# Kernel optimization log

Hardware: AMD Instinct MI355X
Metric: run time of the kernel (lower is better)

## Reference

```python
import jax, jax.numpy as jnp
import numpy as np

THRESHOLD = 1.0


def setup_inputs() -> dict:
    key = jax.random.key(0)
    ks = jax.random.split(key, 7)
    B, D = 262144, 128
    U1, U2 = 64, 32
    return {
        "x": jax.random.normal(ks[0], (B, D), dtype=jnp.float32),
        "W1": jax.random.normal(ks[1], (U1, D), dtype=jnp.float32) * 0.05,
        "b1": jax.random.normal(ks[2], (U1,), dtype=jnp.float32) * 0.05,
        "W2": jax.random.normal(ks[3], (U2, D), dtype=jnp.float32) * 0.05,
        "b2": jax.random.normal(ks[4], (U2,), dtype=jnp.float32) * 0.05,
        "Wf": jax.random.normal(ks[5], (D, U1), dtype=jnp.float32) * 0.05,
        "bf": jax.random.normal(ks[6], (D,), dtype=jnp.float32) * 0.05,
    }


def reference(x, W1, b1, W2, b2, Wf, bf):
    # Per-sample routing decision: mean |x_i| > threshold -> branch1 else branch2
    mask = jnp.mean(jnp.abs(x), axis=1) > THRESHOLD  # (B,)
    o1 = jax.nn.relu(x @ W1.T + b1)                  # (B, 64)
    o2 = jax.nn.relu(x @ W2.T + b2)                  # (B, 32)
    final_dim = W1.shape[0]                          # max(64, 32) = 64
    o2p = jnp.pad(o2, ((0, 0), (0, final_dim - o2.shape[1])))  # zero-pad to final_dim
    branch_out = jnp.where(mask[:, None], o1, o2p)   # (B, 64)
    return branch_out @ Wf.T + bf                    # (B, 128)
```

## Files before the change

### kernel.cpp

```cpp
#include <hip/hip_runtime.h>
#include <stdint.h>

#define FLAG_THRESH 127.0f

typedef short bfrag __attribute__((ext_vector_type(8)));
typedef float floatx4 __attribute__((ext_vector_type(4)));
typedef int intx4 __attribute__((ext_vector_type(4)));

__device__ __forceinline__ unsigned bf16pk(float a, float b) {
    unsigned ua = __float_as_uint(a), ub = __float_as_uint(b);
    ua = (ua + 0x7fffu + ((ua >> 16) & 1u)) >> 16;
    ub = (ub + 0x7fffu + ((ub >> 16) & 1u)) & 0xffff0000u;
    return ua | ub;
}
__device__ __forceinline__ unsigned short bf16s(float a) {
    unsigned ua = __float_as_uint(a);
    return (unsigned short)((ua + 0x7fffu + ((ua >> 16) & 1u)) >> 16);
}
__device__ __forceinline__ bfrag mkfrag(unsigned a, unsigned b, unsigned c, unsigned d) {
    intx4 v = {(int)a, (int)b, (int)c, (int)d};
    return __builtin_bit_cast(bfrag, v);
}
__device__ __forceinline__ void lds_fence_wave() {
    __builtin_amdgcn_wave_barrier();
    __builtin_amdgcn_s_waitcnt(0xc07f);
    __builtin_amdgcn_wave_barrier();
}

__global__ __launch_bounds__(256, 4)
void dyn_main(const float* __restrict__ x, const float* __restrict__ W1,
              const float* __restrict__ b1, const float* __restrict__ W2,
              const float* __restrict__ b2, const float* __restrict__ Wf,
              const float* __restrict__ bf, float* __restrict__ out,
              int ntiles)
{
    __shared__ __align__(16) short w2f[8][64][8];
    __shared__ __align__(16) short wff[8][64][8];
    __shared__ __align__(16) float bfl[128];
    __shared__ __align__(16) short hbuf[4][16 * 40];
    __shared__ __align__(16) float xr[4][128];
    __shared__ __align__(16) float hh[4][64];

    const int tid  = threadIdx.x;
    const int wave = tid >> 6, lane = tid & 63;
    const int l15  = lane & 15, q = lane >> 4;

    for (int idx = tid; idx < 4096; idx += 256) {
        const int j = idx & 7, ln = (idx >> 3) & 63, blk = idx >> 9;
        const int ks = blk >> 1, nb = blk & 1;
        const int u = nb * 16 + (ln & 15);
        const int k = ks * 32 + ((ln >> 4) << 3) + j;
        ((short*)w2f)[idx] = (short)bf16s(W2[u * 128 + k]);
        const int d = blk * 16 + (ln & 15);
        const int c = ((ln >> 4) << 3) + j;
        ((short*)wff)[idx] = (short)bf16s(Wf[d * 64 + c]);
    }
    for (int i = tid; i < 128; i += 256) bfl[i] = bf[i];
    const float b2r0 = b2[l15], b2r1 = b2[16 + l15];
    __syncthreads();

    const unsigned ov = (l15 == 0) ? 0x3f803f80u : 0u;
    const bfrag onesf = mkfrag(ov, ov, ov, ov);

    const int wid = blockIdx.x * 4 + wave;
    const int wstride = gridDim.x * 4;

    long long cur = wid;
    bool more = cur < ntiles;
    floatx4 xl[8];
    if (more) {
        const float* base = x + cur * 2048 + l15 * 128 + q * 8;
        #pragma unroll
        for (int ks = 0; ks < 4; ++ks) {
            xl[2 * ks]     = *(const floatx4*)(base + ks * 32);
            xl[2 * ks + 1] = *(const floatx4*)(base + ks * 32 + 4);
        }
    }

    while (more) {
        const long long nxt = cur + wstride;
        const bool hasnxt = nxt < ntiles;
        floatx4 xc[8];
        #pragma unroll
        for (int i = 0; i < 8; ++i) xc[i] = xl[i];
        if (hasnxt) {
            const float* base = x + nxt * 2048 + l15 * 128 + q * 8;
            #pragma unroll
            for (int ks = 0; ks < 4; ++ks) {
                xl[2 * ks]     = *(const floatx4*)(base + ks * 32);
                xl[2 * ks + 1] = *(const floatx4*)(base + ks * 32 + 4);
            }
        }

        floatx4 a0 = {0.f, 0.f, 0.f, 0.f}, a1 = a0, asum = a0;
        #pragma unroll
        for (int ks = 0; ks < 4; ++ks) {
            const floatx4 p = xc[2 * ks], r = xc[2 * ks + 1];
            const unsigned u0 = bf16pk(p[0], p[1]), u1 = bf16pk(p[2], p[3]);
            const unsigned u2 = bf16pk(r[0], r[1]), u3 = bf16pk(r[2], r[3]);
            const bfrag af = mkfrag(u0, u1, u2, u3);
            const bfrag aa = mkfrag(u0 & 0x7fff7fffu, u1 & 0x7fff7fffu,
                                    u2 & 0x7fff7fffu, u3 & 0x7fff7fffu);
            const bfrag w0 = *(const bfrag*)&w2f[ks * 2 + 0][lane][0];
            const bfrag w1 = *(const bfrag*)&w2f[ks * 2 + 1][lane][0];
            a0   = __builtin_amdgcn_mfma_f32_16x16x32_bf16(af, w0, a0, 0, 0, 0);
            a1   = __builtin_amdgcn_mfma_f32_16x16x32_bf16(af, w1, a1, 0, 0, 0);
            asum = __builtin_amdgcn_mfma_f32_16x16x32_bf16(aa, onesf, asum, 0, 0, 0);
        }

        unsigned rowmask = 0;
        #pragma unroll
        for (int reg = 0; reg < 4; ++reg) {
            const unsigned long long bm =
                __ballot(l15 == 0 && asum[reg] > FLAG_THRESH);
            rowmask |= (unsigned)( bm        & 1ull) << (0 + reg);
            rowmask |= (unsigned)((bm >> 16) & 1ull) << (4 + reg);
            rowmask |= (unsigned)((bm >> 32) & 1ull) << (8 + reg);
            rowmask |= (unsigned)((bm >> 48) & 1ull) << (12 + reg);
        }

        if (__builtin_expect(rowmask != 0, 0)) {
            unsigned m = rowmask;
            while (m) {
                const int r = (int)__builtin_ctz(m); m &= m - 1;
                if (l15 == r) {
                    #pragma unroll
                    for (int ks = 0; ks < 4; ++ks) {
                        *(floatx4*)&xr[wave][ks * 32 + q * 8]     = xc[2 * ks];
                        *(floatx4*)&xr[wave][ks * 32 + q * 8 + 4] = xc[2 * ks + 1];
                    }
                }
                lds_fence_wave();
                const float e0 = xr[wave][lane * 2], e1 = xr[wave][lane * 2 + 1];
                float s = fabsf(e0) + fabsf(e1);
                #pragma unroll
                for (int d = 1; d < 64; d <<= 1) s += __shfl_xor(s, d);
                float hv = 0.f;
                if (s > 128.0f) {
                    float a = 0.f;
                    for (int k = 0; k < 128; k += 4) {
                        const float4 qq = *(const float4*)&xr[wave][k];
                        const float4 wv = *(const float4*)&W1[lane * 128 + k];
                        a = fmaf(qq.x, wv.x, a); a = fmaf(qq.y, wv.y, a);
                        a = fmaf(qq.z, wv.z, a); a = fmaf(qq.w, wv.w, a);
                    }
                    hv = fmaxf(a + b1[lane], 0.f);
                } else if (lane < 32) {
                    float a = 0.f;
                    for (int k = 0; k < 128; k += 4) {
                        const float4 qq = *(const float4*)&xr[wave][k];
                        const float4 wv = *(const float4*)&W2[lane * 128 + k];
                        a = fmaf(qq.x, wv.x, a); a = fmaf(qq.y, wv.y, a);
                        a = fmaf(qq.z, wv.z, a); a = fmaf(qq.w, wv.w, a);
                    }
                    hv = fmaxf(a + b2[lane], 0.f);
                }
                hh[wave][lane] = hv;
                lds_fence_wave();
                #pragma unroll
                for (int jj = 0; jj < 2; ++jj) {
                    const int d = lane + 64 * jj;
                    float a = bf[d];
                    for (int u = 0; u < 64; ++u)
                        a = fmaf(hh[wave][u], Wf[d * 64 + u], a);
                    out[(cur * 16 + r) * 128 + d] = a;
                }
                lds_fence_wave();
            }
        }

        short* hb = &hbuf[wave][0];
        #pragma unroll
        for (int reg = 0; reg < 4; ++reg) {
            const int row = q * 4 + reg;
            hb[row * 40 + l15]      = (short)bf16s(fmaxf(a0[reg] + b2r0, 0.f));
            hb[row * 40 + 16 + l15] = (short)bf16s(fmaxf(a1[reg] + b2r1, 0.f));
        }

        lds_fence_wave();

        const bfrag hfrag = *(const bfrag*)&hb[l15 * 40 + q * 8];
        floatx4 o[8];
        #pragma unroll
        for (int mb = 0; mb < 8; ++mb) o[mb] = (floatx4){0.f, 0.f, 0.f, 0.f};
        #pragma unroll
        for (int mb = 0; mb < 8; ++mb) {
            const bfrag wfr = *(const bfrag*)&wff[mb][lane][0];
            o[mb] = __builtin_amdgcn_mfma_f32_16x16x32_bf16(wfr, hfrag, o[mb], 0, 0, 0);
        }

        float* obase = out + (cur * 16 + l15) * 128 + q * 4;
        if (__builtin_expect(rowmask == 0, 1)) {
            #pragma unroll
            for (int mb = 0; mb < 8; ++mb) {
                const floatx4 bv = *(const floatx4*)&bfl[mb * 16 + q * 4];
                const floatx4 v = o[mb] + bv;
                *(floatx4*)(obase + mb * 16) = v;
            }
        } else {
            if (((rowmask >> l15) & 1u) == 0u) {
                #pragma unroll
                for (int mb = 0; mb < 8; ++mb) {
                    const floatx4 bv = *(const floatx4*)&bfl[mb * 16 + q * 4];
                    const floatx4 v = o[mb] + bv;
                    *(floatx4*)(obase + mb * 16) = v;
                }
            }
        }

        lds_fence_wave();
        cur = nxt; more = hasnxt;
    }
}

extern "C" void kernel_launch(void* const* d_in, const int* in_sizes, int n_in,
                              void* d_out, int out_size, void* d_ws, size_t ws_size,
                              hipStream_t stream) {
    const float* x  = (const float*)d_in[0];
    const float* W1 = (const float*)d_in[1];
    const float* b1 = (const float*)d_in[2];
    const float* W2 = (const float*)d_in[3];
    const float* b2 = (const float*)d_in[4];
    const float* Wf = (const float*)d_in[5];
    const float* bf = (const float*)d_in[6];
    float* out = (float*)d_out;
    (void)d_ws; (void)ws_size;

    const int B = in_sizes[0] / 128;
    const int ntiles = B / 16;

    hipLaunchKernelGGL(dyn_main, dim3(1024), dim3(256), 0, stream,
                       x, W1, b1, W2, b2, Wf, bf, out, ntiles);
}
```

Measured before the change: 262.2 us.

## Stream x tiles into swizzled LDS via async global_load_lds double buffering

Replaces register prefetch of x with direct global-to-LDS 16-byte async loads into a per-wave double buffer using an XOR swizzle, with explicit vmcnt waits. Blocks grow to 512 threads (8 waves) and the grid shrinks to 256 blocks. The fallback path for rows above the threshold now reads x from the LDS buffer, and the bf16 output is always written first and then overwritten for flagged rows. This frees VGPRs and aims to keep more loads in flight, at the cost of 128KB+ of LDS per block, which limits occupancy, and an extra store for flagged rows.

```diff
diff --git a/kernel.cpp b/kernel.cpp
--- a/kernel.cpp
+++ b/kernel.cpp
@@ -27,25 +27,41 @@
     __builtin_amdgcn_wave_barrier();
 }
 
-__global__ __launch_bounds__(256, 4)
+#define VM0  0x0F70
+#define VM8  0x0F78
+#define VM16 0x4F70
+#define WAITVM(imm) do {                       \
+    asm volatile("" ::: "memory");             \
+    __builtin_amdgcn_s_waitcnt(imm);           \
+    asm volatile("" ::: "memory");             \
+    __builtin_amdgcn_sched_barrier(0);         \
+} while (0)
+
+__device__ __forceinline__ void gl16(const void* gsrc, void* ldst) {
+    __builtin_amdgcn_global_load_lds(
+        (const __attribute__((address_space(1))) unsigned int*)gsrc,
+        (__attribute__((address_space(3))) unsigned int*)ldst, 16, 0, 0);
+}
+
+__global__ __launch_bounds__(512, 2)
 void dyn_main(const float* __restrict__ x, const float* __restrict__ W1,
               const float* __restrict__ b1, const float* __restrict__ W2,
               const float* __restrict__ b2, const float* __restrict__ Wf,
               const float* __restrict__ bf, float* __restrict__ out,
               int ntiles)
 {
+    __shared__ __align__(16) float xbuf[8][2][2048];
     __shared__ __align__(16) short w2f[8][64][8];
     __shared__ __align__(16) short wff[8][64][8];
     __shared__ __align__(16) float bfl[128];
-    __shared__ __align__(16) short hbuf[4][16 * 40];
-    __shared__ __align__(16) float xr[4][128];
-    __shared__ __align__(16) float hh[4][64];
+    __shared__ __align__(16) short hbuf[8][16 * 40];
+    __shared__ __align__(16) float hh[8][64];
 
     const int tid  = threadIdx.x;
     const int wave = tid >> 6, lane = tid & 63;
     const int l15  = lane & 15, q = lane >> 4;
 
-    for (int idx = tid; idx < 4096; idx += 256) {
+    for (int idx = tid; idx < 4096; idx += 512) {
         const int j = idx & 7, ln = (idx >> 3) & 63, blk = idx >> 9;
         const int ks = blk >> 1, nb = blk & 1;
         const int u = nb * 16 + (ln & 15);
@@ -55,47 +71,51 @@
         const int c = ((ln >> 4) << 3) + j;
         ((short*)wff)[idx] = (short)bf16s(Wf[d * 64 + c]);
     }
-    for (int i = tid; i < 128; i += 256) bfl[i] = bf[i];
+    for (int i = tid; i < 128; i += 512) bfl[i] = bf[i];
     const float b2r0 = b2[l15], b2r1 = b2[16 + l15];
     __syncthreads();
 
     const unsigned ov = (l15 == 0) ? 0x3f803f80u : 0u;
     const bfrag onesf = mkfrag(ov, ov, ov, ov);
 
-    const int wid = blockIdx.x * 4 + wave;
-    const int wstride = gridDim.x * 4;
+    const int wid = blockIdx.x * 8 + wave;
+    const int wstride = gridDim.x * 8;
+
+#define ISSUE_TILE(t, b) do {                                              \
+        const char* gb_ = (const char*)(x + (long long)(t) * 2048);        \
+        char* lb_ = (char*)&xbuf[wave][(b)][0];                            \
+        _Pragma("unroll")                                                  \
+        for (int j_ = 0; j_ < 8; ++j_) {                                   \
+            const int off_ = j_ * 1024 + lane * 16;                        \
+            const int src_ = off_ ^ (((off_ >> 9) & 7) << 4);              \
+            gl16(gb_ + src_, lb_ + j_ * 1024);                             \
+        }                                                                  \
+        __builtin_amdgcn_sched_barrier(0);                                 \
+    } while (0)
 
     long long cur = wid;
     bool more = cur < ntiles;
-    floatx4 xl[8];
-    if (more) {
-        const float* base = x + cur * 2048 + l15 * 128 + q * 8;
-        #pragma unroll
-        for (int ks = 0; ks < 4; ++ks) {
-            xl[2 * ks]     = *(const floatx4*)(base + ks * 32);
-            xl[2 * ks + 1] = *(const floatx4*)(base + ks * 32 + 4);
-        }
-    }
+    int bufc = 0;
+    if (more) ISSUE_TILE(cur, 0);
+    bool first = true;
 
     while (more) {
         const long long nxt = cur + wstride;
         const bool hasnxt = nxt < ntiles;
-        floatx4 xc[8];
-        #pragma unroll
-        for (int i = 0; i < 8; ++i) xc[i] = xl[i];
-        if (hasnxt) {
-            const float* base = x + nxt * 2048 + l15 * 128 + q * 8;
-            #pragma unroll
-            for (int ks = 0; ks < 4; ++ks) {
-                xl[2 * ks]     = *(const floatx4*)(base + ks * 32);
-                xl[2 * ks + 1] = *(const floatx4*)(base + ks * 32 + 4);
-            }
-        }
+        if (hasnxt) ISSUE_TILE(nxt, bufc ^ 1);
+
+        if (first) { if (hasnxt) WAITVM(VM8);  else WAITVM(VM0); }
+        else       { if (hasnxt) WAITVM(VM16); else WAITVM(VM8); }
+
+        const char* xb = (const char*)&xbuf[wave][bufc][0];
+        const int sw = (l15 & 7) << 4;
 
         floatx4 a0 = {0.f, 0.f, 0.f, 0.f}, a1 = a0, asum = a0;
         #pragma unroll
         for (int ks = 0; ks < 4; ++ks) {
-            const floatx4 p = xc[2 * ks], r = xc[2 * ks + 1];
+            const int g0 = (l15 << 9) + (ks << 7) + (q << 5);
+            const floatx4 p = *(const floatx4*)(xb + (g0 ^ sw));
+            const floatx4 r = *(const floatx4*)(xb + ((g0 + 16) ^ sw));
             const unsigned u0 = bf16pk(p[0], p[1]), u1 = bf16pk(p[2], p[3]);
             const unsigned u2 = bf16pk(r[0], r[1]), u3 = bf16pk(r[2], r[3]);
             const bfrag af = mkfrag(u0, u1, u2, u3);
@@ -119,27 +139,51 @@
             rowmask |= (unsigned)((bm >> 48) & 1ull) << (12 + reg);
         }
 
+        short* hb = &hbuf[wave][0];
+        #pragma unroll
+        for (int reg = 0; reg < 4; ++reg) {
+            const int row = q * 4 + reg;
+            hb[row * 40 + l15]      = (short)bf16s(fmaxf(a0[reg] + b2r0, 0.f));
+            hb[row * 40 + 16 + l15] = (short)bf16s(fmaxf(a1[reg] + b2r1, 0.f));
+        }
+
+        lds_fence_wave();
+
+        const bfrag hfrag = *(const bfrag*)&hb[l15 * 40 + q * 8];
+        floatx4 o[8];
+        #pragma unroll
+        for (int mb = 0; mb < 8; ++mb) o[mb] = (floatx4){0.f, 0.f, 0.f, 0.f};
+        #pragma unroll
+        for (int mb = 0; mb < 8; ++mb) {
+            const bfrag wfr = *(const bfrag*)&wff[mb][lane][0];
+            o[mb] = __builtin_amdgcn_mfma_f32_16x16x32_bf16(wfr, hfrag, o[mb], 0, 0, 0);
+        }
+
+        float* obase = out + (cur * 16 + l15) * 128 + q * 4;
+        #pragma unroll
+        for (int mb = 0; mb < 8; ++mb) {
+            const floatx4 bv = *(const floatx4*)&bfl[mb * 16 + q * 4];
+            const floatx4 v = o[mb] + bv;
+            *(floatx4*)(obase + mb * 16) = v;
+        }
+
         if (__builtin_expect(rowmask != 0, 0)) {
-            unsigned m = rowmask;
-            while (m) {
-                const int r = (int)__builtin_ctz(m); m &= m - 1;
-                if (l15 == r) {
-                    #pragma unroll
-                    for (int ks = 0; ks < 4; ++ks) {
-                        *(floatx4*)&xr[wave][ks * 32 + q * 8]     = xc[2 * ks];
-                        *(floatx4*)&xr[wave][ks * 32 + q * 8 + 4] = xc[2 * ks + 1];
-                    }
-                }
-                lds_fence_wave();
-                const float e0 = xr[wave][lane * 2], e1 = xr[wave][lane * 2 + 1];
-                float s = fabsf(e0) + fabsf(e1);
+            WAITVM(VM0);
+            unsigned mm = rowmask;
+            while (mm) {
+                const int r = (int)__builtin_ctz(mm); mm &= mm - 1;
+                const int swr = (r & 7) << 4;
+                const float2 xv =
+                    *(const float2*)(xb + (((r << 9) + lane * 8) ^ swr));
+                float s = fabsf(xv.x) + fabsf(xv.y);
                 #pragma unroll
                 for (int d = 1; d < 64; d <<= 1) s += __shfl_xor(s, d);
                 float hv = 0.f;
                 if (s > 128.0f) {
                     float a = 0.f;
                     for (int k = 0; k < 128; k += 4) {
-                        const float4 qq = *(const float4*)&xr[wave][k];
+                        const float4 qq = *(const float4*)(
+                            xb + (((r << 9) + (k << 2)) ^ swr));
                         const float4 wv = *(const float4*)&W1[lane * 128 + k];
                         a = fmaf(qq.x, wv.x, a); a = fmaf(qq.y, wv.y, a);
                         a = fmaf(qq.z, wv.z, a); a = fmaf(qq.w, wv.w, a);
@@ -148,7 +192,8 @@
                 } else if (lane < 32) {
                     float a = 0.f;
                     for (int k = 0; k < 128; k += 4) {
-                        const float4 qq = *(const float4*)&xr[wave][k];
+                        const float4 qq = *(const float4*)(
+                            xb + (((r << 9) + (k << 2)) ^ swr));
                         const float4 wv = *(const float4*)&W2[lane * 128 + k];
                         a = fmaf(qq.x, wv.x, a); a = fmaf(qq.y, wv.y, a);
                         a = fmaf(qq.z, wv.z, a); a = fmaf(qq.w, wv.w, a);
@@ -169,48 +214,10 @@
             }
         }
 
-        short* hb = &hbuf[wave][0];
-        #pragma unroll
-        for (int reg = 0; reg < 4; ++reg) {
-            const int row = q * 4 + reg;
-            hb[row * 40 + l15]      = (short)bf16s(fmaxf(a0[reg] + b2r0, 0.f));
-            hb[row * 40 + 16 + l15] = (short)bf16s(fmaxf(a1[reg] + b2r1, 0.f));
-        }
-
         lds_fence_wave();
-
-        const bfrag hfrag = *(const bfrag*)&hb[l15 * 40 + q * 8];
-        floatx4 o[8];
-        #pragma unroll
-        for (int mb = 0; mb < 8; ++mb) o[mb] = (floatx4){0.f, 0.f, 0.f, 0.f};
-        #pragma unroll
-        for (int mb = 0; mb < 8; ++mb) {
-            const bfrag wfr = *(const bfrag*)&wff[mb][lane][0];
-            o[mb] = __builtin_amdgcn_mfma_f32_16x16x32_bf16(wfr, hfrag, o[mb], 0, 0, 0);
-        }
-
-        float* obase = out + (cur * 16 + l15) * 128 + q * 4;
-        if (__builtin_expect(rowmask == 0, 1)) {
-            #pragma unroll
-            for (int mb = 0; mb < 8; ++mb) {
-                const floatx4 bv = *(const floatx4*)&bfl[mb * 16 + q * 4];
-                const floatx4 v = o[mb] + bv;
-                *(floatx4*)(obase + mb * 16) = v;
-            }
-        } else {
-            if (((rowmask >> l15) & 1u) == 0u) {
-                #pragma unroll
-                for (int mb = 0; mb < 8; ++mb) {
-                    const floatx4 bv = *(const floatx4*)&bfl[mb * 16 + q * 4];
-                    const floatx4 v = o[mb] + bv;
-                    *(floatx4*)(obase + mb * 16) = v;
-                }
-            }
-        }
-
-        lds_fence_wave();
-        cur = nxt; more = hasnxt;
+        first = false; bufc ^= 1; cur = nxt; more = hasnxt;
     }
+#undef ISSUE_TILE
 }
 
 extern "C" void kernel_launch(void* const* d_in, const int* in_sizes, int n_in,
@@ -229,6 +236,6 @@
     const int B = in_sizes[0] / 128;
     const int ntiles = B / 16;
 
-    hipLaunchKernelGGL(dyn_main, dim3(1024), dim3(256), 0, stream,
+    hipLaunchKernelGGL(dyn_main, dim3(256), dim3(512), 0, stream,
                        x, W1, b1, W2, b2, Wf, bf, out, ntiles);
 }
```

Result: faster. 255.7 us (-2.5%).

## Reorder rare-row fixup after main store, drop LDS staging, raise grid

Applied to the files above, without the earlier changes.

The fast MFMA path now runs unconditionally and writes all 16 rows. Any flagged rows are then recomputed in fp32 and overwritten, with a waitcnt placed first so the earlier stores are ordered before the overwrite. The xr/hh LDS arrays are removed: the fixup reads x directly from global memory and reuses hbuf as scratch, which cuts LDS use and may allow more blocks per CU. The grid grows from a fixed 1024 blocks to up to 2048, sized by tile count, which changes the persistent-block scheduling.

```diff
diff --git a/kernel.cpp b/kernel.cpp
--- a/kernel.cpp
+++ b/kernel.cpp
@@ -38,8 +38,6 @@
     __shared__ __align__(16) short wff[8][64][8];
     __shared__ __align__(16) float bfl[128];
     __shared__ __align__(16) short hbuf[4][16 * 40];
-    __shared__ __align__(16) float xr[4][128];
-    __shared__ __align__(16) float hh[4][64];
 
     const int tid  = threadIdx.x;
     const int wave = tid >> 6, lane = tid & 63;
@@ -119,27 +117,50 @@
             rowmask |= (unsigned)((bm >> 48) & 1ull) << (12 + reg);
         }
 
+        short* hb = &hbuf[wave][0];
+        #pragma unroll
+        for (int reg = 0; reg < 4; ++reg) {
+            const int row = q * 4 + reg;
+            hb[row * 40 + l15]      = (short)bf16s(fmaxf(a0[reg] + b2r0, 0.f));
+            hb[row * 40 + 16 + l15] = (short)bf16s(fmaxf(a1[reg] + b2r1, 0.f));
+        }
+
+        lds_fence_wave();
+
+        const bfrag hfrag = *(const bfrag*)&hb[l15 * 40 + q * 8];
+        floatx4 o[8];
+        #pragma unroll
+        for (int mb = 0; mb < 8; ++mb) o[mb] = (floatx4){0.f, 0.f, 0.f, 0.f};
+        #pragma unroll
+        for (int mb = 0; mb < 8; ++mb) {
+            const bfrag wfr = *(const bfrag*)&wff[mb][lane][0];
+            o[mb] = __builtin_amdgcn_mfma_f32_16x16x32_bf16(wfr, hfrag, o[mb], 0, 0, 0);
+        }
+
+        float* obase = out + (cur * 16 + l15) * 128 + q * 4;
+        #pragma unroll
+        for (int mb = 0; mb < 8; ++mb) {
+            const floatx4 bv = *(const floatx4*)&bfl[mb * 16 + q * 4];
+            const floatx4 v = o[mb] + bv;
+            *(floatx4*)(obase + mb * 16) = v;
+        }
+
         if (__builtin_expect(rowmask != 0, 0)) {
-            unsigned m = rowmask;
-            while (m) {
-                const int r = (int)__builtin_ctz(m); m &= m - 1;
-                if (l15 == r) {
-                    #pragma unroll
-                    for (int ks = 0; ks < 4; ++ks) {
-                        *(floatx4*)&xr[wave][ks * 32 + q * 8]     = xc[2 * ks];
-                        *(floatx4*)&xr[wave][ks * 32 + q * 8 + 4] = xc[2 * ks + 1];
-                    }
-                }
-                lds_fence_wave();
-                const float e0 = xr[wave][lane * 2], e1 = xr[wave][lane * 2 + 1];
-                float s = fabsf(e0) + fabsf(e1);
+            __builtin_amdgcn_s_waitcnt(0x0F70);
+            float* hw = (float*)&hbuf[wave][0];
+            unsigned mm = rowmask;
+            while (mm) {
+                const int r = (int)__builtin_ctz(mm); mm &= mm - 1;
+                const float* xrow = x + (cur * 16 + r) * 128;
+                const float2 xv = *(const float2*)&xrow[lane * 2];
+                float s = fabsf(xv.x) + fabsf(xv.y);
                 #pragma unroll
                 for (int d = 1; d < 64; d <<= 1) s += __shfl_xor(s, d);
                 float hv = 0.f;
                 if (s > 128.0f) {
                     float a = 0.f;
                     for (int k = 0; k < 128; k += 4) {
-                        const float4 qq = *(const float4*)&xr[wave][k];
+                        const float4 qq = *(const float4*)&xrow[k];
                         const float4 wv = *(const float4*)&W1[lane * 128 + k];
                         a = fmaf(qq.x, wv.x, a); a = fmaf(qq.y, wv.y, a);
                         a = fmaf(qq.z, wv.z, a); a = fmaf(qq.w, wv.w, a);
@@ -148,63 +169,24 @@
                 } else if (lane < 32) {
                     float a = 0.f;
                     for (int k = 0; k < 128; k += 4) {
-                        const float4 qq = *(const float4*)&xr[wave][k];
+                        const float4 qq = *(const float4*)&xrow[k];
                         const float4 wv = *(const float4*)&W2[lane * 128 + k];
                         a = fmaf(qq.x, wv.x, a); a = fmaf(qq.y, wv.y, a);
                         a = fmaf(qq.z, wv.z, a); a = fmaf(qq.w, wv.w, a);
                     }
                     hv = fmaxf(a + b2[lane], 0.f);
                 }
-                hh[wave][lane] = hv;
+                hw[lane] = hv;
                 lds_fence_wave();
                 #pragma unroll
                 for (int jj = 0; jj < 2; ++jj) {
                     const int d = lane + 64 * jj;
                     float a = bf[d];
                     for (int u = 0; u < 64; ++u)
-                        a = fmaf(hh[wave][u], Wf[d * 64 + u], a);
+                        a = fmaf(hw[u], Wf[d * 64 + u], a);
                     out[(cur * 16 + r) * 128 + d] = a;
                 }
                 lds_fence_wave();
-            }
-        }
-
-        short* hb = &hbuf[wave][0];
-        #pragma unroll
-        for (int reg = 0; reg < 4; ++reg) {
-            const int row = q * 4 + reg;
-            hb[row * 40 + l15]      = (short)bf16s(fmaxf(a0[reg] + b2r0, 0.f));
-            hb[row * 40 + 16 + l15] = (short)bf16s(fmaxf(a1[reg] + b2r1, 0.f));
-        }
-
-        lds_fence_wave();
-
-        const bfrag hfrag = *(const bfrag*)&hb[l15 * 40 + q * 8];
-        floatx4 o[8];
-        #pragma unroll
-        for (int mb = 0; mb < 8; ++mb) o[mb] = (floatx4){0.f, 0.f, 0.f, 0.f};
-        #pragma unroll
-        for (int mb = 0; mb < 8; ++mb) {
-            const bfrag wfr = *(const bfrag*)&wff[mb][lane][0];
-            o[mb] = __builtin_amdgcn_mfma_f32_16x16x32_bf16(wfr, hfrag, o[mb], 0, 0, 0);
-        }
-
-        float* obase = out + (cur * 16 + l15) * 128 + q * 4;
-        if (__builtin_expect(rowmask == 0, 1)) {
-            #pragma unroll
-            for (int mb = 0; mb < 8; ++mb) {
-                const floatx4 bv = *(const floatx4*)&bfl[mb * 16 + q * 4];
-                const floatx4 v = o[mb] + bv;
-                *(floatx4*)(obase + mb * 16) = v;
-            }
-        } else {
-            if (((rowmask >> l15) & 1u) == 0u) {
-                #pragma unroll
-                for (int mb = 0; mb < 8; ++mb) {
-                    const floatx4 bv = *(const floatx4*)&bfl[mb * 16 + q * 4];
-                    const floatx4 v = o[mb] + bv;
-                    *(floatx4*)(obase + mb * 16) = v;
-                }
             }
         }
 
@@ -229,6 +211,9 @@
     const int B = in_sizes[0] / 128;
     const int ntiles = B / 16;
 
-    hipLaunchKernelGGL(dyn_main, dim3(1024), dim3(256), 0, stream,
+    int nblk = (ntiles + 3) / 4;
+    if (nblk > 2048) nblk = 2048;
+    if (nblk < 1) nblk = 1;
+    hipLaunchKernelGGL(dyn_main, dim3(nblk), dim3(256), 0, stream,
                        x, W1, b1, W2, b2, Wf, bf, out, ntiles);
 }
```

Result: faster. 255.0 us (-2.7%).
